# Kernel tuning notes

Measured on AMD Instinct MI355X. Metric: run time of the kernel, lower is better.

## Reference

```python
import jax, jax.numpy as jnp
import numpy as np

DIM = 64
NUM_HEAD = 4
C_IN = 2 * DIM                      # dim * proj_ratio
N_PER_HEAD = C_IN // NUM_HEAD       # 32
M_TRI = N_PER_HEAD * (N_PER_HEAD + 1) // 2   # 528
C_POOL = NUM_HEAD * M_TRI           # 2112 == dim*(dim+2)/2
EPS = 1e-5


def setup_inputs() -> dict:
    key = jax.random.key(0)
    ks = jax.random.split(key, 8)
    B, H, W = 4, 128, 128
    x = jax.random.normal(ks[0], (B, C_IN, H, W), dtype=jnp.float32)
    norm1_w = 1.0 + 0.1 * jax.random.normal(ks[1], (C_IN,), dtype=jnp.float32)
    norm1_b = 0.1 * jax.random.normal(ks[2], (C_IN,), dtype=jnp.float32)
    dr_w = 0.02 * jax.random.normal(ks[3], (DIM, C_POOL), dtype=jnp.float32)
    dr_b = 0.02 * jax.random.normal(ks[4], (DIM,), dtype=jnp.float32)
    norm2_w = 1.0 + 0.1 * jax.random.normal(ks[5], (DIM,), dtype=jnp.float32)
    norm2_b = 0.1 * jax.random.normal(ks[6], (DIM,), dtype=jnp.float32)
    fc1_w = 0.05 * jax.random.normal(ks[7], (DIM, DIM), dtype=jnp.float32)
    fc1_b = jnp.zeros((DIM,), dtype=jnp.float32)
    return {"x": x, "norm1_w": norm1_w, "norm1_b": norm1_b,
            "dr_w": dr_w, "dr_b": dr_b,
            "norm2_w": norm2_w, "norm2_b": norm2_b,
            "fc1_w": fc1_w, "fc1_b": fc1_b}


def _layernorm_nchw(x, g, b):
    # LayerNorm over channel dim of NCHW tensor (torch permutes to NHWC first)
    xt = jnp.transpose(x, (0, 2, 3, 1))
    mu = jnp.mean(xt, axis=-1, keepdims=True)
    var = jnp.mean(jnp.square(xt - mu), axis=-1, keepdims=True)
    y = (xt - mu) / jnp.sqrt(var + EPS) * g + b
    return jnp.transpose(y, (0, 3, 1, 2))


def reference(x, norm1_w, norm1_b, dr_w, dr_b, norm2_w, norm2_b, fc1_w, fc1_b):
    B, C, H, W = x.shape
    L = H * W
    nh, n = NUM_HEAD, N_PER_HEAD

    # --- norm1 ---
    x = _layernorm_nchw(x, norm1_w, norm1_b)

    # --- MHSP ---
    # channel shuffle: group = C // num_head = n, group_C = num_head
    x = x.reshape(B, n, nh, H, W).transpose(0, 2, 1, 3, 4).reshape(B, C, H, W)
    # unfold with kernel=1, stride=1, pad=0 is a pure reshape -> [B, L, C]
    t = x.reshape(B, C, L).transpose(0, 2, 1).reshape(B, L, nh, n)
    # per-position per-head rank-1 outer product: [B, L, nh, n, n]
    outer = jnp.einsum('blhi,blhj->blhij', t, t)
    # sparse_mapping matmul == gather of upper-triangle entries (row-major i<=j)
    iu, ju = np.triu_indices(n)
    pf = outer[..., iu, ju]                      # [B, L, nh, m]
    pf = pf.reshape(B, L, nh * M_TRI).transpose(0, 2, 1).reshape(B, C_POOL, H, W)

    # --- CTM token mixer ---
    C2 = C_POOL
    y = pf.reshape(B, nh, C2 // nh, L)
    yn = y / jnp.linalg.norm(y, axis=2, keepdims=True)
    mid = L // 2
    x0 = yn[..., mid]                            # [B, nh, C2/nh]
    attn = jnp.einsum('bhc,bhcl->bhl', x0, yn)   # [B, nh, L]
    attn = jax.nn.softmax(attn, axis=-1)[:, :, None, :]
    y = (y * attn * float(L)).reshape(B, C2, H, W)

    # --- dimension reduction (1x1 conv) ---
    z = jnp.einsum('bchw,oc->bohw', y, dr_w) + dr_b[None, :, None, None]

    # --- norm2 + LightMlp (1x1 conv + GELU) ---
    z = _layernorm_nchw(z, norm2_w, norm2_b)
    z = jnp.einsum('bchw,oc->bohw', z, fc1_w) + fc1_b[None, :, None, None]
    z = jax.nn.gelu(z, approximate=False)
    return z
```

## Files before the change

### kernel.cpp

```cpp
#include <hip/hip_runtime.h>
#include <hip/hip_bf16.h>
#include <math.h>

#define B_    4
#define CIN   128
#define L_    16384
#define NH    4
#define NN    32
#define MT    528
#define CP    2112
#define DIM_  64
#define LT    64
#define MID   8192
#define EPS_  1e-5f

#define KPH   640
#define KTOT  2560
#define WSWN  (KTOT * DIM_)
#define FSWN  (2 * 4 * 64 * 8)
#define LOGITS_BLOCKS 1024
#define PREP_BLOCKS   656

typedef __attribute__((ext_vector_type(8))) short short8;
typedef __attribute__((ext_vector_type(4))) float float4v;
typedef __attribute__((ext_vector_type(4))) unsigned uint4v;
typedef __attribute__((ext_vector_type(2))) _Float16 h2;
typedef __attribute__((ext_vector_type(8))) _Float16 half8;

__device__ inline unsigned short f2h(float f) {
  _Float16 h = (_Float16)f;
  return __builtin_bit_cast(unsigned short, h);
}

__device__ inline h2 pkrtz(float a, float b) {
  return __builtin_bit_cast(h2, __builtin_amdgcn_cvt_pkrtz(a, b));
}

__device__ inline void kb_decode(int id, int& i, int& jb) {
  if (id < 32)      { i = id >> 2;               jb = id & 3; }
  else if (id < 56) { int r = id - 32; int d = r / 3; i = 8 + d;  jb = 1 + (r - 3 * d); }
  else if (id < 72) { int r = id - 56; i = 16 + (r >> 1); jb = 2 + (r & 1); }
  else              { i = 24 + (id - 72);         jb = 3; }
}

__global__ __launch_bounds__(256) void k_pre(const float* __restrict__ dr_w,
                                             const float* __restrict__ fc1_w,
                                             const float* __restrict__ x,
                                             const float* __restrict__ g1,
                                             const float* __restrict__ b1,
                                             unsigned short* __restrict__ wsw,
                                             unsigned short* __restrict__ fsw,
                                             float* __restrict__ ws_a,
                                             float* __restrict__ ws_bsum) {
  if (blockIdx.x >= LOGITS_BLOCKS) {
    int s = (blockIdx.x - LOGITS_BLOCKS) * 256 + threadIdx.x;
    if (s < WSWN) {
      int j    = s & 7;
      int lane = (s >> 3) & 63;
      int ot   = (s >> 9) & 3;
      int ksg  = s >> 11;
      int o  = ot * 16 + (lane & 15);
      int h  = lane >> 4;
      int i, jb; kb_decode(ksg, i, jb);
      int jch = jb * 8 + j;
      float val = 0.f;
      if (jch >= i) {
        int fi = 32 * i - (i * (i - 1)) / 2;
        int m  = h * MT + fi + (jch - i);
        val = dr_w[(size_t)o * CP + m];
      }
      wsw[s] = f2h(val);
    } else {
      int s2 = s - WSWN;
      int j    = s2 & 7;
      int lane = (s2 >> 3) & 63;
      int ot   = (s2 >> 9) & 3;
      int ks2  = s2 >> 11;
      int o = ot * 16 + (lane & 15);
      int c = ks2 * 32 + (lane >> 4) * 8 + j;
      fsw[s2] = f2h(fc1_w[o * DIM_ + c]);
    }
    return;
  }
  int blk = blockIdx.x;
  int b = blk >> 8;
  int l0 = (blk & 255) << 6;
  int t = threadIdx.x;
  int l = t & 63, q = t >> 6;
  __shared__ float xs[CIN], smid[CIN];
  __shared__ float part[4][64], part2[4][64], mu_s[64], isd_s[64];
  __shared__ float musd[2];

  if (t < CIN) xs[t] = x[(size_t)b * CIN * L_ + (size_t)t * L_ + MID];

  float tv[32];
  const float* xb = x + (size_t)b * CIN * L_ + l0 + l;
  float s = 0.f, s2 = 0.f;
#pragma unroll
  for (int cc = 0; cc < 32; cc++) {
    float v = xb[(size_t)(cc * 4 + q) * L_];
    tv[cc] = v; s += v; s2 += v * v;
  }
  part[q][l] = s; part2[q][l] = s2;
  __syncthreads();
  if (t < 64) {
    float a = xs[t], bb = xs[t + 64];
    float ms = a + bb, ms2 = a * a + bb * bb;
#pragma unroll
    for (int mk = 1; mk < 64; mk <<= 1) {
      ms += __shfl_xor(ms, mk, 64);
      ms2 += __shfl_xor(ms2, mk, 64);
    }
    if (t == 0) {
      float mu = ms * (1.f / CIN);
      musd[0] = mu;
      musd[1] = rsqrtf(ms2 * (1.f / CIN) - mu * mu + EPS_);
    }
    float su = part[0][t] + part[1][t] + part[2][t] + part[3][t];
    float su2 = part2[0][t] + part2[1][t] + part2[2][t] + part2[3][t];
    float mu = su * (1.f / CIN);
    float var = su2 * (1.f / CIN) - mu * mu;
    mu_s[t] = mu; isd_s[t] = rsqrtf(var + EPS_);
  }
  __syncthreads();
  if (t < CIN) {
    int c = ((t & 31) << 2) + (t >> 5);
    smid[t] = (xs[c] - musd[0]) * musd[1] * g1[c] + b1[c];
  }
  {
    float mu = mu_s[l], isd = isd_s[l];
#pragma unroll
    for (int cc = 0; cc < 32; cc++) {
      int co = cc * 4 + q;
      tv[cc] = (tv[cc] - mu) * isd * g1[co] + b1[co];
    }
  }
  __syncthreads();
  float T2 = 0.f, T4 = 0.f, st = 0.f, sc2 = 0.f, S2 = 0.f, S4 = 0.f;
#pragma unroll
  for (int i = 0; i < 32; i++) {
    float si = smid[q * 32 + i];
    float ti = tv[i];
    float t2 = ti * ti;
    T2 += t2; T4 = fmaf(t2, t2, T4);
    float ci = si * ti;
    st += ci; sc2 = fmaf(ci, ci, sc2);
    float s2i = si * si;
    S2 += s2i; S4 = fmaf(s2i, s2i, S4);
  }
  float num = 0.5f * (st * st + sc2);
  float logit = num * rsqrtf(0.25f * (T2 * T2 + T4) * (S2 * S2 + S4));
  float e = expf(logit - 1.f);
  ws_a[((size_t)b * NH + q) * L_ + l0 + l] = e;
  float ws = e;
#pragma unroll
  for (int mk = 1; mk < 64; mk <<= 1) ws += __shfl_xor(ws, mk, 64);
  if (l == 0) ws_bsum[((size_t)b * NH + q) * 256 + (blk & 255)] = ws;
}

struct __align__(16) SmemM {
  union __align__(16) { unsigned short p2[4 * 5 * 4 * 16 * 8]; float zb[64 * 65]; } u1;
  unsigned short zn2[4 * 2 * 4 * 16 * 8];
  float part[4][64], part2[4][64], mu_s[64], isd_s[64];
};

__global__ __launch_bounds__(256) void k_main(const float* __restrict__ x,
      const float* __restrict__ g1, const float* __restrict__ b1,
      const float* __restrict__ dr_b,
      const float* __restrict__ g2, const float* __restrict__ b2,
      const float* __restrict__ fc1_b,
      const unsigned short* __restrict__ wsw, const unsigned short* __restrict__ fsw,
      const float* __restrict__ ws_a, const float* __restrict__ ws_bsum,
      float* __restrict__ out) {
  __shared__ SmemM sm;
  int blk = blockIdx.x;
  int b = blk >> 8;
  int l0 = (blk & 255) << 6;
  int t = threadIdx.x;
  int l = t & 63, q = t >> 6;

  float asum;
  {
    const float* bs = ws_bsum + ((size_t)b * NH + q) * 256;
    float a0 = bs[l] + bs[l + 64] + bs[l + 128] + bs[l + 192];
#pragma unroll
    for (int mk = 1; mk < 64; mk <<= 1) a0 += __shfl_xor(a0, mk, 64);
    asum = a0;
  }
  float e = ws_a[((size_t)b * NH + q) * L_ + l0 + l];
  float sa = sqrtf(e * ((float)L_ / asum));

  const float* xb = x + (size_t)b * CIN * L_ + l0 + l;
  h2 tnh[16];
  float s = 0.f, s2 = 0.f;
#pragma unroll
  for (int r = 0; r < 16; r++) {
    float v0 = xb[(size_t)((2 * r) * 4 + q) * L_];
    float v1 = xb[(size_t)((2 * r + 1) * 4 + q) * L_];
    s += v0 + v1; s2 += v0 * v0 + v1 * v1;
    tnh[r] = pkrtz(v0, v1);
  }
  sm.part[q][l] = s; sm.part2[q][l] = s2;
  __syncthreads();
  if (t < 64) {
    float su = sm.part[0][t] + sm.part[1][t] + sm.part[2][t] + sm.part[3][t];
    float su2 = sm.part2[0][t] + sm.part2[1][t] + sm.part2[2][t] + sm.part2[3][t];
    float mu = su * (1.f / CIN);
    float var = su2 * (1.f / CIN) - mu * mu;
    sm.mu_s[t] = mu; sm.isd_s[t] = rsqrtf(var + EPS_);
  }
  __syncthreads();
  {
    float mu = sm.mu_s[l], isd = sm.isd_s[l];
#pragma unroll
    for (int r = 0; r < 16; r++) {
      int c0 = (2 * r) * 4 + q, c1 = c0 + 4;
      float v0 = ((float)tnh[r][0] - mu) * isd * g1[c0] + b1[c0];
      float v1 = ((float)tnh[r][1] - mu) * isd * g1[c1] + b1[c1];
      v0 *= sa; v1 *= sa;
      tnh[r] = pkrtz(v0, v1);
    }
  }

  const int otp = q & 1, ltp = q >> 1;
  const int lta = ltp * 2, ltb = ltp * 2 + 1;
  float4v acc[2][2];
  acc[0][0] = (float4v)0.f; acc[0][1] = (float4v)0.f;
  acc[1][0] = (float4v)0.f; acc[1][1] = (float4v)0.f;
  int tl = l;
  int ltile = l >> 4, n = l & 15;

#pragma unroll
  for (int p = 0; p < 16; p++) {
#pragma unroll
    for (int ks = 0; ks < 5; ks++) {
      const int g = p * 5 + ks;
      int i, jb; kb_decode(g, i, jb);
      _Float16 uh = tnh[i >> 1][i & 1];
      h2 uu = {uh, uh};
      h2 p0 = uu * tnh[jb * 4 + 0];
      h2 p1 = uu * tnh[jb * 4 + 1];
      h2 p2v = uu * tnh[jb * 4 + 2];
      h2 p3 = uu * tnh[jb * 4 + 3];
      uint4v pv = {__builtin_bit_cast(unsigned, p0), __builtin_bit_cast(unsigned, p1),
                   __builtin_bit_cast(unsigned, p2v), __builtin_bit_cast(unsigned, p3)};
      *(uint4v*)&sm.u1.p2[(((ltile * 5 + ks) * 4 + q) * 16 + n) * 8] = pv;
    }
    __syncthreads();
#pragma unroll
    for (int ks = 0; ks < 5; ks++) {
      const unsigned short* wk = wsw + (size_t)(p * 5 + ks) * 2048 + otp * 1024 + tl * 8;
      half8 a0 = *(const half8*)(wk);
      half8 a1 = *(const half8*)(wk + 512);
      half8 b0 = *(half8*)&sm.u1.p2[((lta * 5 + ks) * 64 + tl) * 8];
      half8 b1v = *(half8*)&sm.u1.p2[((ltb * 5 + ks) * 64 + tl) * 8];
      acc[0][0] = __builtin_amdgcn_mfma_f32_16x16x32_f16(a0, b0,  acc[0][0], 0, 0, 0);
      acc[0][1] = __builtin_amdgcn_mfma_f32_16x16x32_f16(a0, b1v, acc[0][1], 0, 0, 0);
      acc[1][0] = __builtin_amdgcn_mfma_f32_16x16x32_f16(a1, b0,  acc[1][0], 0, 0, 0);
      acc[1][1] = __builtin_amdgcn_mfma_f32_16x16x32_f16(a1, b1v, acc[1][1], 0, 0, 0);
    }
    __syncthreads();
  }

  int quad = tl >> 4;
#pragma unroll
  for (int oi = 0; oi < 2; oi++) {
#pragma unroll
    for (int li = 0; li < 2; li++) {
      int ot = otp * 2 + oi, ltx = ltp * 2 + li;
#pragma unroll
      for (int r = 0; r < 4; r++) {
        int o = ot * 16 + quad * 4 + r;
        sm.u1.zb[(ltx * 16 + n) * 65 + o] = acc[oi][li][r] + dr_b[o];
      }
    }
  }
  __syncthreads();
  {
    float ss = 0.f, ss2 = 0.f;
#pragma unroll
    for (int k = 0; k < 16; k++) {
      float v = sm.u1.zb[l * 65 + q * 16 + k];
      ss += v; ss2 += v * v;
    }
    sm.part[q][l] = ss; sm.part2[q][l] = ss2;
  }
  __syncthreads();
  if (t < 64) {
    float su = sm.part[0][t] + sm.part[1][t] + sm.part[2][t] + sm.part[3][t];
    float su2 = sm.part2[0][t] + sm.part2[1][t] + sm.part2[2][t] + sm.part2[3][t];
    float mu = su * (1.f / DIM_);
    float var = su2 * (1.f / DIM_) - mu * mu;
    sm.mu_s[t] = mu; sm.isd_s[t] = rsqrtf(var + EPS_);
  }
  __syncthreads();
  {
    float mu2 = sm.mu_s[l], isd2 = sm.isd_s[l];
#pragma unroll
    for (int kk = 0; kk < 2; kk++) {
      int kb2 = q * 2 + kk;
      int c0 = kb2 * 8;
      unsigned short pk[8];
#pragma unroll
      for (int e8 = 0; e8 < 8; e8++) {
        int c = c0 + e8;
        float v = (sm.u1.zb[l * 65 + c] - mu2) * isd2 * g2[c] + b2[c];
        pk[e8] = f2h(v);
      }
      int ks2 = kb2 >> 2, qd2 = kb2 & 3;
      *(short8*)&sm.zn2[(((ltile * 2 + ks2) * 4 + qd2) * 16 + n) * 8] = *(short8*)pk;
    }
  }
  __syncthreads();
  float4v acc2[4];
  acc2[0] = (float4v)0.f; acc2[1] = (float4v)0.f; acc2[2] = (float4v)0.f; acc2[3] = (float4v)0.f;
#pragma unroll
  for (int ks2 = 0; ks2 < 2; ks2++) {
    half8 bz = *(half8*)&sm.zn2[((q * 2 + ks2) * 64 + tl) * 8];
    const unsigned short* fk = fsw + ks2 * 2048 + tl * 8;
    half8 f0 = *(const half8*)(fk);
    half8 f1 = *(const half8*)(fk + 512);
    half8 f2 = *(const half8*)(fk + 1024);
    half8 f3 = *(const half8*)(fk + 1536);
    acc2[0] = __builtin_amdgcn_mfma_f32_16x16x32_f16(f0, bz, acc2[0], 0, 0, 0);
    acc2[1] = __builtin_amdgcn_mfma_f32_16x16x32_f16(f1, bz, acc2[1], 0, 0, 0);
    acc2[2] = __builtin_amdgcn_mfma_f32_16x16x32_f16(f2, bz, acc2[2], 0, 0, 0);
    acc2[3] = __builtin_amdgcn_mfma_f32_16x16x32_f16(f3, bz, acc2[3], 0, 0, 0);
  }
#pragma unroll
  for (int ot = 0; ot < 4; ot++) {
#pragma unroll
    for (int r = 0; r < 4; r++) {
      int o2 = ot * 16 + quad * 4 + r;
      float sv = acc2[ot][r] + fc1_b[o2];
      float g = 0.5f * sv * (1.f + erff(sv * 0.70710678118f));
      out[((size_t)b * DIM_ + o2) * L_ + l0 + q * 16 + n] = g;
    }
  }
}

extern "C" void kernel_launch(void* const* d_in, const int* in_sizes, int n_in,
                              void* d_out, int out_size, void* d_ws, size_t ws_size,
                              hipStream_t stream) {
  const float* x    = (const float*)d_in[0];
  const float* n1w  = (const float*)d_in[1];
  const float* n1b  = (const float*)d_in[2];
  const float* drw  = (const float*)d_in[3];
  const float* drb  = (const float*)d_in[4];
  const float* n2w  = (const float*)d_in[5];
  const float* n2b  = (const float*)d_in[6];
  const float* fc1w = (const float*)d_in[7];
  const float* fc1b = (const float*)d_in[8];
  float* out = (float*)d_out;
  float* ws = (float*)d_ws;
  float* ws_a    = ws;
  float* ws_bsum = ws_a + (size_t)B_ * NH * L_;
  unsigned short* wsw = (unsigned short*)(ws_bsum + B_ * NH * 256);
  unsigned short* fsw = wsw + WSWN;

  hipLaunchKernelGGL(k_pre, dim3(LOGITS_BLOCKS + PREP_BLOCKS), dim3(256), 0, stream,
                     drw, fc1w, x, n1w, n1b, wsw, fsw, ws_a, ws_bsum);
  hipLaunchKernelGGL(k_main, dim3(B_ * (L_ / LT)), dim3(256), 0, stream,
                     x, n1w, n1b, drb, n2w, n2b, fc1b, wsw, fsw, ws_a, ws_bsum, out);
}
```

Baseline: 128.3 us.

## Fuse attention-logit pass into main kernel with atomic grid-wide softmax-sum barrier

Moves the per-position attention logit computation from the prep kernel into the main kernel, removing a second full read of x and the stored per-position exp values. The softmax denominator is accumulated with global atomics per batch and head, and each block spin-waits on a counter until all 256 blocks of its batch have contributed. This saves memory traffic and a launch phase, but relies on all blocks being co-resident to avoid deadlock and adds barrier stall time. Logits are now computed from fp16-rounded normalized values.

```diff
diff --git a/kernel.cpp b/kernel.cpp
--- a/kernel.cpp
+++ b/kernel.cpp
@@ -18,8 +18,8 @@
 #define KTOT  2560
 #define WSWN  (KTOT * DIM_)
 #define FSWN  (2 * 4 * 64 * 8)
-#define LOGITS_BLOCKS 1024
 #define PREP_BLOCKS   656
+
 
 typedef __attribute__((ext_vector_type(8))) short short8;
 typedef __attribute__((ext_vector_type(4))) float float4v;
@@ -45,122 +45,50 @@
 
 __global__ __launch_bounds__(256) void k_pre(const float* __restrict__ dr_w,
                                              const float* __restrict__ fc1_w,
-                                             const float* __restrict__ x,
-                                             const float* __restrict__ g1,
-                                             const float* __restrict__ b1,
                                              unsigned short* __restrict__ wsw,
                                              unsigned short* __restrict__ fsw,
-                                             float* __restrict__ ws_a,
-                                             float* __restrict__ ws_bsum) {
-  if (blockIdx.x >= LOGITS_BLOCKS) {
-    int s = (blockIdx.x - LOGITS_BLOCKS) * 256 + threadIdx.x;
-    if (s < WSWN) {
-      int j    = s & 7;
-      int lane = (s >> 3) & 63;
-      int ot   = (s >> 9) & 3;
-      int ksg  = s >> 11;
-      int o  = ot * 16 + (lane & 15);
-      int h  = lane >> 4;
-      int i, jb; kb_decode(ksg, i, jb);
-      int jch = jb * 8 + j;
-      float val = 0.f;
-      if (jch >= i) {
-        int fi = 32 * i - (i * (i - 1)) / 2;
-        int m  = h * MT + fi + (jch - i);
-        val = dr_w[(size_t)o * CP + m];
-      }
-      wsw[s] = f2h(val);
-    } else {
-      int s2 = s - WSWN;
-      int j    = s2 & 7;
-      int lane = (s2 >> 3) & 63;
-      int ot   = (s2 >> 9) & 3;
-      int ks2  = s2 >> 11;
-      int o = ot * 16 + (lane & 15);
-      int c = ks2 * 32 + (lane >> 4) * 8 + j;
-      fsw[s2] = f2h(fc1_w[o * DIM_ + c]);
-    }
-    return;
-  }
-  int blk = blockIdx.x;
-  int b = blk >> 8;
-  int l0 = (blk & 255) << 6;
+                                             float* __restrict__ ws_asum,
+                                             unsigned* __restrict__ ws_cnt) {
   int t = threadIdx.x;
-  int l = t & 63, q = t >> 6;
-  __shared__ float xs[CIN], smid[CIN];
-  __shared__ float part[4][64], part2[4][64], mu_s[64], isd_s[64];
-  __shared__ float musd[2];
-
-  if (t < CIN) xs[t] = x[(size_t)b * CIN * L_ + (size_t)t * L_ + MID];
-
-  float tv[32];
-  const float* xb = x + (size_t)b * CIN * L_ + l0 + l;
-  float s = 0.f, s2 = 0.f;
-#pragma unroll
-  for (int cc = 0; cc < 32; cc++) {
-    float v = xb[(size_t)(cc * 4 + q) * L_];
-    tv[cc] = v; s += v; s2 += v * v;
-  }
-  part[q][l] = s; part2[q][l] = s2;
-  __syncthreads();
-  if (t < 64) {
-    float a = xs[t], bb = xs[t + 64];
-    float ms = a + bb, ms2 = a * a + bb * bb;
-#pragma unroll
-    for (int mk = 1; mk < 64; mk <<= 1) {
-      ms += __shfl_xor(ms, mk, 64);
-      ms2 += __shfl_xor(ms2, mk, 64);
-    }
-    if (t == 0) {
-      float mu = ms * (1.f / CIN);
-      musd[0] = mu;
-      musd[1] = rsqrtf(ms2 * (1.f / CIN) - mu * mu + EPS_);
-    }
-    float su = part[0][t] + part[1][t] + part[2][t] + part[3][t];
-    float su2 = part2[0][t] + part2[1][t] + part2[2][t] + part2[3][t];
-    float mu = su * (1.f / CIN);
-    float var = su2 * (1.f / CIN) - mu * mu;
-    mu_s[t] = mu; isd_s[t] = rsqrtf(var + EPS_);
-  }
-  __syncthreads();
-  if (t < CIN) {
-    int c = ((t & 31) << 2) + (t >> 5);
-    smid[t] = (xs[c] - musd[0]) * musd[1] * g1[c] + b1[c];
-  }
-  {
-    float mu = mu_s[l], isd = isd_s[l];
-#pragma unroll
-    for (int cc = 0; cc < 32; cc++) {
-      int co = cc * 4 + q;
-      tv[cc] = (tv[cc] - mu) * isd * g1[co] + b1[co];
-    }
-  }
-  __syncthreads();
-  float T2 = 0.f, T4 = 0.f, st = 0.f, sc2 = 0.f, S2 = 0.f, S4 = 0.f;
-#pragma unroll
-  for (int i = 0; i < 32; i++) {
-    float si = smid[q * 32 + i];
-    float ti = tv[i];
-    float t2 = ti * ti;
-    T2 += t2; T4 = fmaf(t2, t2, T4);
-    float ci = si * ti;
-    st += ci; sc2 = fmaf(ci, ci, sc2);
-    float s2i = si * si;
-    S2 += s2i; S4 = fmaf(s2i, s2i, S4);
-  }
-  float num = 0.5f * (st * st + sc2);
-  float logit = num * rsqrtf(0.25f * (T2 * T2 + T4) * (S2 * S2 + S4));
-  float e = expf(logit - 1.f);
-  ws_a[((size_t)b * NH + q) * L_ + l0 + l] = e;
-  float ws = e;
-#pragma unroll
-  for (int mk = 1; mk < 64; mk <<= 1) ws += __shfl_xor(ws, mk, 64);
-  if (l == 0) ws_bsum[((size_t)b * NH + q) * 256 + (blk & 255)] = ws;
+  if (blockIdx.x == 0 && t < 2 * B_ * NH) {
+    if (t < B_ * NH) ws_asum[t] = 0.f;
+    else             ws_cnt[t - B_ * NH] = 0u;
+  }
+  int s = blockIdx.x * 256 + t;
+  if (s < WSWN) {
+    int j    = s & 7;
+    int lane = (s >> 3) & 63;
+    int ot   = (s >> 9) & 3;
+    int ksg  = s >> 11;
+    int o  = ot * 16 + (lane & 15);
+    int h  = lane >> 4;
+    int i, jb; kb_decode(ksg, i, jb);
+    int jch = jb * 8 + j;
+    float val = 0.f;
+    if (jch >= i) {
+      int fi = 32 * i - (i * (i - 1)) / 2;
+      int m  = h * MT + fi + (jch - i);
+      val = dr_w[(size_t)o * CP + m];
+    }
+    wsw[s] = f2h(val);
+  } else {
+    int s2 = s - WSWN;
+    int j    = s2 & 7;
+    int lane = (s2 >> 3) & 63;
+    int ot   = (s2 >> 9) & 3;
+    int ks2  = s2 >> 11;
+    int o = ot * 16 + (lane & 15);
+    int c = ks2 * 32 + (lane >> 4) * 8 + j;
+    fsw[s2] = f2h(fc1_w[o * DIM_ + c]);
+  }
 }
 
 struct __align__(16) SmemM {
   union __align__(16) { unsigned short p2[4 * 5 * 4 * 16 * 8]; float zb[64 * 65]; } u1;
-  unsigned short zn2[4 * 2 * 4 * 16 * 8];
+  union __align__(16) {
+    unsigned short zn2[4 * 2 * 4 * 16 * 8];
+    struct { float xs[CIN]; float smid[CIN]; float musd[2]; } ph1;
+  } u2;
   float part[4][64], part2[4][64], mu_s[64], isd_s[64];
 };
 
@@ -170,7 +98,7 @@
       const float* __restrict__ g2, const float* __restrict__ b2,
       const float* __restrict__ fc1_b,
       const unsigned short* __restrict__ wsw, const unsigned short* __restrict__ fsw,
-      const float* __restrict__ ws_a, const float* __restrict__ ws_bsum,
+      float* __restrict__ ws_asum, unsigned* __restrict__ ws_cnt,
       float* __restrict__ out) {
   __shared__ SmemM sm;
   int blk = blockIdx.x;
@@ -179,17 +107,7 @@
   int t = threadIdx.x;
   int l = t & 63, q = t >> 6;
 
-  float asum;
-  {
-    const float* bs = ws_bsum + ((size_t)b * NH + q) * 256;
-    float a0 = bs[l] + bs[l + 64] + bs[l + 128] + bs[l + 192];
-#pragma unroll
-    for (int mk = 1; mk < 64; mk <<= 1) a0 += __shfl_xor(a0, mk, 64);
-    asum = a0;
-  }
-  float e = ws_a[((size_t)b * NH + q) * L_ + l0 + l];
-  float sa = sqrtf(e * ((float)L_ / asum));
-
+  if (t < CIN) sm.u2.ph1.xs[t] = x[(size_t)b * CIN * L_ + (size_t)t * L_ + MID];
   const float* xb = x + (size_t)b * CIN * L_ + l0 + l;
   h2 tnh[16];
   float s = 0.f, s2 = 0.f;
@@ -203,6 +121,18 @@
   sm.part[q][l] = s; sm.part2[q][l] = s2;
   __syncthreads();
   if (t < 64) {
+    float a = sm.u2.ph1.xs[t], bb = sm.u2.ph1.xs[t + 64];
+    float ms = a + bb, ms2 = a * a + bb * bb;
+#pragma unroll
+    for (int mk = 1; mk < 64; mk <<= 1) {
+      ms += __shfl_xor(ms, mk, 64);
+      ms2 += __shfl_xor(ms2, mk, 64);
+    }
+    if (t == 0) {
+      float mu = ms * (1.f / CIN);
+      sm.u2.ph1.musd[0] = mu;
+      sm.u2.ph1.musd[1] = rsqrtf(ms2 * (1.f / CIN) - mu * mu + EPS_);
+    }
     float su = sm.part[0][t] + sm.part[1][t] + sm.part[2][t] + sm.part[3][t];
     float su2 = sm.part2[0][t] + sm.part2[1][t] + sm.part2[2][t] + sm.part2[3][t];
     float mu = su * (1.f / CIN);
@@ -210,6 +140,10 @@
     sm.mu_s[t] = mu; sm.isd_s[t] = rsqrtf(var + EPS_);
   }
   __syncthreads();
+  if (t < CIN) {
+    int c = ((t & 31) << 2) + (t >> 5);
+    sm.u2.ph1.smid[t] = (sm.u2.ph1.xs[c] - sm.u2.ph1.musd[0]) * sm.u2.ph1.musd[1] * g1[c] + b1[c];
+  }
   {
     float mu = sm.mu_s[l], isd = sm.isd_s[l];
 #pragma unroll
@@ -217,10 +151,54 @@
       int c0 = (2 * r) * 4 + q, c1 = c0 + 4;
       float v0 = ((float)tnh[r][0] - mu) * isd * g1[c0] + b1[c0];
       float v1 = ((float)tnh[r][1] - mu) * isd * g1[c1] + b1[c1];
-      v0 *= sa; v1 *= sa;
       tnh[r] = pkrtz(v0, v1);
     }
   }
+  __syncthreads();
+  float e;
+  {
+    float T2 = 0.f, T4 = 0.f, st = 0.f, sc2 = 0.f, S2 = 0.f, S4 = 0.f;
+#pragma unroll
+    for (int i = 0; i < 32; i++) {
+      float si = sm.u2.ph1.smid[q * 32 + i];
+      float ti = (float)tnh[i >> 1][i & 1];
+      float t2 = ti * ti;
+      T2 += t2; T4 = fmaf(t2, t2, T4);
+      float ci = si * ti;
+      st += ci; sc2 = fmaf(ci, ci, sc2);
+      float s2i = si * si;
+      S2 += s2i; S4 = fmaf(s2i, s2i, S4);
+    }
+    float num = 0.5f * (st * st + sc2);
+    float logit = num * rsqrtf(0.25f * (T2 * T2 + T4) * (S2 * S2 + S4));
+    e = expf(logit - 1.f);
+  }
+  {
+    float wsum = e;
+#pragma unroll
+    for (int mk = 1; mk < 64; mk <<= 1) wsum += __shfl_xor(wsum, mk, 64);
+    if (l == 0) {
+      atomicAdd(&ws_asum[b * NH + q], wsum);
+      __threadfence();
+      atomicAdd(&ws_cnt[b * NH + q], 1u);
+    }
+  }
+  if (t == 0) {
+    unsigned base = b * NH;
+    for (;;) {
+      unsigned tot = atomicOr(&ws_cnt[base + 0], 0u) + atomicOr(&ws_cnt[base + 1], 0u)
+                   + atomicOr(&ws_cnt[base + 2], 0u) + atomicOr(&ws_cnt[base + 3], 0u);
+      if (tot >= 4u * 256u) break;
+      __builtin_amdgcn_s_sleep(16);
+    }
+#pragma unroll
+    for (int i = 0; i < 4; i++) sm.part[0][i] = atomicAdd(&ws_asum[base + i], 0.f);
+  }
+  __syncthreads();
+  float sa = sqrtf(e * ((float)L_ / sm.part[0][q]));
+#pragma unroll
+  for (int r = 0; r < 16; r++)
+    tnh[r] = pkrtz((float)tnh[r][0] * sa, (float)tnh[r][1] * sa);
 
   const int otp = q & 1, ltp = q >> 1;
   const int lta = ltp * 2, ltb = ltp * 2 + 1;
@@ -308,7 +286,7 @@
         pk[e8] = f2h(v);
       }
       int ks2 = kb2 >> 2, qd2 = kb2 & 3;
-      *(short8*)&sm.zn2[(((ltile * 2 + ks2) * 4 + qd2) * 16 + n) * 8] = *(short8*)pk;
+      *(short8*)&sm.u2.zn2[(((ltile * 2 + ks2) * 4 + qd2) * 16 + n) * 8] = *(short8*)pk;
     }
   }
   __syncthreads();
@@ -316,7 +294,7 @@
   acc2[0] = (float4v)0.f; acc2[1] = (float4v)0.f; acc2[2] = (float4v)0.f; acc2[3] = (float4v)0.f;
 #pragma unroll
   for (int ks2 = 0; ks2 < 2; ks2++) {
-    half8 bz = *(half8*)&sm.zn2[((q * 2 + ks2) * 64 + tl) * 8];
+    half8 bz = *(half8*)&sm.u2.zn2[((q * 2 + ks2) * 64 + tl) * 8];
     const unsigned short* fk = fsw + ks2 * 2048 + tl * 8;
     half8 f0 = *(const half8*)(fk);
     half8 f1 = *(const half8*)(fk + 512);
@@ -353,13 +331,13 @@
   const float* fc1b = (const float*)d_in[8];
   float* out = (float*)d_out;
   float* ws = (float*)d_ws;
-  float* ws_a    = ws;
-  float* ws_bsum = ws_a + (size_t)B_ * NH * L_;
-  unsigned short* wsw = (unsigned short*)(ws_bsum + B_ * NH * 256);
+  float*    ws_asum = ws;
+  unsigned* ws_cnt  = (unsigned*)(ws + B_ * NH);
+  unsigned short* wsw = (unsigned short*)(ws + 2 * B_ * NH);
   unsigned short* fsw = wsw + WSWN;
 
-  hipLaunchKernelGGL(k_pre, dim3(LOGITS_BLOCKS + PREP_BLOCKS), dim3(256), 0, stream,
-                     drw, fc1w, x, n1w, n1b, wsw, fsw, ws_a, ws_bsum);
+  hipLaunchKernelGGL(k_pre, dim3(PREP_BLOCKS), dim3(256), 0, stream,
+                     drw, fc1w, wsw, fsw, ws_asum, ws_cnt);
   hipLaunchKernelGGL(k_main, dim3(B_ * (L_ / LT)), dim3(256), 0, stream,
-                     x, n1w, n1b, drb, n2w, n2b, fc1b, wsw, fsw, ws_a, ws_bsum, out);
-}
+                     x, n1w, n1b, drb, n2w, n2b, fc1b, wsw, fsw, ws_asum, ws_cnt, out);
+}
```

Result: slower. 479.2 us (+273.4%).
